# Optimization experiments

Hardware: AMD Instinct MI355X
Metric: run time of the kernel (lower is better)

Reference implementation:

```python
import jax, jax.numpy as jnp
import numpy as np
import math

N, LQ, DIM = 4, 1000, 256
HEADS, DHEAD, DEPTH = 8, 32, 2
LVLS, NPTS, MLP = 5, 4, 512
SCALE = DHEAD ** -0.5
SHAPES = np.array([[128, 128], [64, 64], [32, 32], [16, 16], [8, 8]], np.int32)
AREAS = SHAPES[:, 0] * SHAPES[:, 1]
STARTS = np.concatenate([[0], np.cumsum(AREAS)[:-1]]).astype(np.int32)
LIN = int(AREAS.sum())


def _ln(x, g, b):
    m = jnp.mean(x, -1, keepdims=True)
    v = jnp.var(x, -1, keepdims=True)
    return (x - m) * jax.lax.rsqrt(v + 1e-5) * g + b


def _gelu(x):  # tanh-approx GELU exactly as the torch module
    c = math.sqrt(2.0 / math.pi)
    return 0.5 * x * (1.0 + jnp.tanh(c * (x + 0.044715 * x ** 3)))


def _ms_deform(value, shapes, starts, loc, aw):
    # value [N,Lin,H,D]; loc [N,Lq,H,L,P,2] normalized to [0,1]; aw [N,Lq,H,L,P]
    n, lq, h, L, p, _ = loc.shape
    d = value.shape[-1]
    ni = jnp.arange(n)[:, None, None, None]
    hi = jnp.arange(h)[None, None, :, None]
    out = jnp.zeros((n, lq, h, d), value.dtype)
    for l in range(L):  # fixed small pyramid depth
        Hl, Wl = int(shapes[l, 0]), int(shapes[l, 1])
        s = int(starts[l])
        v = value[:, s:s + Hl * Wl].reshape(n, Hl, Wl, h, d)
        gx = loc[:, :, :, l, :, 0] * Wl - 0.5  # [N,Lq,H,P]
        gy = loc[:, :, :, l, :, 1] * Hl - 0.5
        x0 = jnp.floor(gx); y0 = jnp.floor(gy)
        lx = gx - x0; ly = gy - y0
        x0i = x0.astype(jnp.int32); y0i = y0.astype(jnp.int32)
        def corner(yi, xi):
            ok = ((yi >= 0) & (yi < Hl) & (xi >= 0) & (xi < Wl)).astype(value.dtype)
            g = v[ni, jnp.clip(yi, 0, Hl - 1), jnp.clip(xi, 0, Wl - 1), hi]  # [N,Lq,H,P,D]
            return g * ok[..., None]
        samp = (corner(y0i, x0i) * ((1 - ly) * (1 - lx))[..., None]
                + corner(y0i, x0i + 1) * ((1 - ly) * lx)[..., None]
                + corner(y0i + 1, x0i) * (ly * (1 - lx))[..., None]
                + corner(y0i + 1, x0i + 1) * (ly * lx)[..., None])
        out = out + jnp.einsum('nqhp,nqhpd->nqhd', aw[:, :, :, l], samp)
    return out.reshape(n, lq, h * d)


def _forward(x, src, center_pos, pos_w, pos_b, ln1_g, ln1_b, qkv_w, out_w, out_b,
             ln2_g, ln2_b, off_w, off_b, aw_w, aw_b, val_w, val_b, op_w, op_b,
             ln3_g, ln3_b, ff_w1, ff_b1, ff_w2, ff_b2, spatial_shapes, level_start_index):
    shapes = np.asarray(spatial_shapes)
    starts = np.asarray(level_start_index)
    n, lq, dim = x.shape
    pe = center_pos @ pos_w + pos_b                                   # pos_embedding(center_pos)
    ref = jnp.broadcast_to(center_pos[:, :, None, :], (n, lq, LVLS, 2))
    onorm = jnp.asarray(np.stack([shapes[:, 1], shapes[:, 0]], -1), x.dtype)  # [L,2] = (W,H)
    for i in range(DEPTH):
        # --- self-attention: PreNorm(x + pe) ---
        xn = _ln(x + pe, ln1_g[i], ln1_b[i])
        qkv = xn @ qkv_w[i]
        q, k, v = jnp.split(qkv, 3, axis=-1)
        q = q.reshape(n, lq, HEADS, DHEAD).transpose(0, 2, 1, 3)
        k = k.reshape(n, lq, HEADS, DHEAD).transpose(0, 2, 1, 3)
        v = v.reshape(n, lq, HEADS, DHEAD).transpose(0, 2, 1, 3)
        att = jax.nn.softmax(jnp.einsum('nhid,nhjd->nhij', q, k) * SCALE, axis=-1)
        o = jnp.einsum('nhij,nhjd->nhid', att, v).transpose(0, 2, 1, 3).reshape(n, lq, HEADS * DHEAD)
        x = x + o @ out_w[i] + out_b[i]
        # --- deformable cross-attention: PreNorm_CA norms query and src with same LN ---
        xn = _ln(x, ln2_g[i], ln2_b[i])
        srcn = _ln(src, ln2_g[i], ln2_b[i])
        query = xn + pe
        value = (srcn @ val_w[i] + val_b[i]).reshape(n, -1, HEADS, DHEAD)
        off = (query @ off_w[i] + off_b[i]).reshape(n, lq, HEADS, LVLS, NPTS, 2)
        aw = jax.nn.softmax((query @ aw_w[i] + aw_b[i]).reshape(n, lq, HEADS, LVLS * NPTS), axis=-1)
        aw = aw.reshape(n, lq, HEADS, LVLS, NPTS)
        loc = ref[:, :, None, :, None, :] + off / onorm[None, None, None, :, None, :]
        o = _ms_deform(value, shapes, starts, loc, aw)
        x = x + o @ op_w[i] + op_b[i]
        # --- feedforward: PreNorm ---
        xn = _ln(x, ln3_g[i], ln3_b[i])
        x = x + _gelu(xn @ ff_w1[i] + ff_b1[i]) @ ff_w2[i] + ff_b2[i]
    return x


def setup_inputs() -> dict:
    key = jax.random.key(0)
    ks = iter(jax.random.split(key, 64))
    r = lambda sh, s=0.02: jax.random.normal(next(ks), sh, jnp.float32) * s
    # sampling_offsets bias grid init (as in MSDeformAttn._reset_parameters)
    thetas = np.arange(HEADS) * (2.0 * math.pi / HEADS)
    grid = np.stack([np.cos(thetas), np.sin(thetas)], -1)
    grid = grid / np.abs(grid).max(-1, keepdims=True)
    grid = np.tile(grid[:, None, None, :], (1, LVLS, NPTS, 1)) * (np.arange(NPTS) + 1)[None, None, :, None]
    off_b = jnp.tile(jnp.asarray(grid.reshape(-1), jnp.float32)[None], (DEPTH, 1))
    return dict(
        x=jax.random.normal(next(ks), (N, LQ, DIM), jnp.float32),
        src=jax.random.normal(next(ks), (N, LIN, DIM), jnp.float32),
        center_pos=jax.random.uniform(next(ks), (N, LQ, 2), jnp.float32),
        spatial_shapes=jnp.asarray(SHAPES),
        level_start_index=jnp.asarray(STARTS),
        pos_w=r((2, DIM), 0.5), pos_b=jnp.zeros((DIM,), jnp.float32),
        ln1_g=jnp.ones((DEPTH, DIM), jnp.float32), ln1_b=jnp.zeros((DEPTH, DIM), jnp.float32),
        qkv_w=r((DEPTH, DIM, 3 * HEADS * DHEAD)),
        out_w=r((DEPTH, HEADS * DHEAD, DIM)), out_b=jnp.zeros((DEPTH, DIM), jnp.float32),
        ln2_g=jnp.ones((DEPTH, DIM), jnp.float32), ln2_b=jnp.zeros((DEPTH, DIM), jnp.float32),
        off_w=r((DEPTH, DIM, HEADS * LVLS * NPTS * 2)), off_b=off_b,
        aw_w=r((DEPTH, DIM, HEADS * LVLS * NPTS)), aw_b=jnp.zeros((DEPTH, HEADS * LVLS * NPTS), jnp.float32),
        val_w=r((DEPTH, DIM, HEADS * DHEAD)), val_b=jnp.zeros((DEPTH, HEADS * DHEAD), jnp.float32),
        op_w=r((DEPTH, HEADS * DHEAD, DIM)), op_b=jnp.zeros((DEPTH, DIM), jnp.float32),
        ln3_g=jnp.ones((DEPTH, DIM), jnp.float32), ln3_b=jnp.zeros((DEPTH, DIM), jnp.float32),
        ff_w1=r((DEPTH, DIM, MLP)), ff_b1=jnp.zeros((DEPTH, MLP), jnp.float32),
        ff_w2=r((DEPTH, MLP, DIM)), ff_b2=jnp.zeros((DEPTH, DIM), jnp.float32),
    )


def reference(x, src, center_pos, spatial_shapes, level_start_index, pos_w, pos_b,
              ln1_g, ln1_b, qkv_w, out_w, out_b, ln2_g, ln2_b, off_w, off_b,
              aw_w, aw_b, val_w, val_b, op_w, op_b, ln3_g, ln3_b,
              ff_w1, ff_b1, ff_w2, ff_b2):
    return _forward(x, src, center_pos, pos_w, pos_b, ln1_g, ln1_b, qkv_w, out_w, out_b,
                    ln2_g, ln2_b, off_w, off_b, aw_w, aw_b, val_w, val_b, op_w, op_b,
                    ln3_g, ln3_b, ff_w1, ff_b1, ff_w2, ff_b2, spatial_shapes, level_start_index)
```

## Files before the change

### kernel.cpp

```cpp
#include <hip/hip_runtime.h>
#include <hip/hip_bf16.h>
#include <math.h>

#define DIM 256
#define NB 4
#define LQ 1000
#define MLPD 512
#define LIN 21824
#define ROWS_X 4000
#define ROWS_SRC 87296
#define ATT_SCALE 0.17677669529663687f
#define LDK 72

typedef __hip_bfloat16 bf16;
typedef __attribute__((ext_vector_type(8))) short short8;
typedef __attribute__((ext_vector_type(4))) float floatx4;

__device__ __forceinline__ float rdv(const void* p, int f, size_t i){
    if (f) return ((const float*)p)[i];
    unsigned u = ((unsigned)((const unsigned short*)p)[i]) << 16;
    union { unsigned u; float f; } c; c.u = u; return c.f;
}
__device__ __forceinline__ short f2bs(float v){
    bf16 h = __float2bfloat16(v);
    return *reinterpret_cast<short*>(&h);
}
__device__ __forceinline__ float bs2f(short s){
// ... 5 lines not shown
    int t = threadIdx.x;
    bool hit = false;
    #pragma unroll
    for (int k = 0; k < 4; ++k) {
        unsigned short b = u[(t*4 + k)*2];
        union { unsigned u; float f; } c; c.u = ((unsigned)b) << 16;
        if (!(fabsf(c.f) <= 1000.f)) hit = true;
    }
    unsigned long long m = __ballot(hit);
    __shared__ unsigned long long red[4];
    if ((t & 63) == 0) red[t >> 6] = m;
    __syncthreads();
    if (t == 0) flag[0] = ((red[0]|red[1]|red[2]|red[3]) != 0ULL) ? 1 : 0;
}

struct PTab { const void* src[15]; float* dst[15]; int n[15]; };
__global__ void convs_kernel(PTab t, const int* __restrict__ flag){
    int j = blockIdx.y;
    int i = blockIdx.x*256 + threadIdx.x;
    if (i >= t.n[j]) return;
    t.dst[j][i] = t.src[j] ? rdv(t.src[j], flag[0], i) : 0.f;
}

__global__ void catb_kernel(const void* __restrict__ offb, const void* __restrict__ awb,
                            const int* __restrict__ flag, float* __restrict__ oab){
    int f = flag[0];
    int layer = blockIdx.y;
    int idx = blockIdx.x*256 + threadIdx.x;
    if (idx >= 480) return;
    float v = (idx < 320) ? rdv(offb, f, (size_t)layer*320 + idx)
                          : rdv(awb,  f, (size_t)layer*160 + idx - 320);
    oab[layer*480 + idx] = v;
}

struct WT { const void* src[8]; short* dst[8]; const float* scl[8];
            int K[8]; int N[8]; int ld[8]; int ro[8]; };
__global__ void wtransall_kernel(WT t, const int* __restrict__ flag){
    int j = blockIdx.z >> 1, b = blockIdx.z & 1;
    int K = t.K[j], N = t.N[j];
    int k0 = blockIdx.x*32, n0 = blockIdx.y*32;
    if (k0 >= K || n0 >= N) return;
    int f = flag[0];
    __shared__ float tt[32][33];
    int tx = threadIdx.x & 31, ty = threadIdx.x >> 5;
    size_t base = (size_t)b * K * N;
    for (int i = ty; i < 32; i += 8) {
        int k = k0 + i, n = n0 + tx;
// ... 26 lines not shown
    float part = t.bv[j][(size_t)b*256 + k] *
                 rdv(t.W[j], f, (size_t)b*256*N + (size_t)k*N + n);
    #pragma unroll
    for (int o = 32; o; o >>= 1) part += __shfl_xor(part, o, 64);
    __shared__ float red[4];
    int wave = k >> 6, lane = k & 63;
    if (lane == 0) red[wave] = part;
    __syncthreads();
    if (k == 0) {
        float s = red[0] + red[1] + red[2] + red[3];
        if (t.base[j]) s += t.base[j][(size_t)b*N + n];
        t.dst[j][(size_t)b*N + n] = s;
    }
}

__global__ void pe_kernel(const void* __restrict__ cp, const void* __restrict__ pw,
                          const void* __restrict__ pb, const int* __restrict__ flag,
                          float* __restrict__ pe){
    int f = flag[0];
    int row = blockIdx.x, t = threadIdx.x;
    float cx = rdv(cp, f, (size_t)row*2);
    float cy = rdv(cp, f, (size_t)row*2 + 1);
    pe[(size_t)row*DIM + t] = cx*rdv(pw, f, t) + cy*rdv(pw, f, DIM + t) + rdv(pb, f, t);
}

__global__ __launch_bounds__(256) void convx_kernel(const void* __restrict__ x,
        const float* __restrict__ pe, const int* __restrict__ flag,
        float* __restrict__ xf, float2* __restrict__ st){
    int f = flag[0];
    int wave = threadIdx.x >> 6, lane = threadIdx.x & 63;
    int row = blockIdx.x*4 + wave;
    float4 v;
    if (f) v = *(const float4*)((const float*)x + (size_t)row*DIM + lane*4);
    else {
        ushort4 u = *(const ushort4*)((const unsigned short*)x + (size_t)row*DIM + lane*4);
        v = make_float4(bs2f((short)u.x), bs2f((short)u.y), bs2f((short)u.z), bs2f((short)u.w));
    }
    *(float4*)(xf + (size_t)row*DIM + lane*4) = v;
    float4 p = *(const float4*)(pe + (size_t)row*DIM + lane*4);
    float a0 = v.x+p.x, a1 = v.y+p.y, a2 = v.z+p.z, a3 = v.w+p.w;
    float s  = a0+a1+a2+a3;
    float s2 = a0*a0+a1*a1+a2*a2+a3*a3;
    #pragma unroll
    for (int o = 32; o; o >>= 1) {
        s  += __shfl_xor(s,  o, 64);
        s2 += __shfl_xor(s2, o, 64);
    }
    if (lane == 0) st[row] = make_float2(s, s2);
}

__global__ __launch_bounds__(256) void stats2n_kernel(const void* __restrict__ src,
                                                      const int* __restrict__ flag,
                                                      bf16* __restrict__ srcn){
    int f = flag[0];
    int wave = threadIdx.x >> 6, lane = threadIdx.x & 63;
    int row = blockIdx.x*4 + wave;
    float v0, v1, v2, v3;
    if (f) {
        float4 x = *(const float4*)((const float*)src + (size_t)row*DIM + lane*4);
        v0 = x.x; v1 = x.y; v2 = x.z; v3 = x.w;
    } else {
        ushort4 u = *(const ushort4*)((const unsigned short*)src + (size_t)row*DIM + lane*4);
        v0 = bs2f((short)u.x); v1 = bs2f((short)u.y);
        v2 = bs2f((short)u.z); v3 = bs2f((short)u.w);
    }
    float s  = v0 + v1 + v2 + v3;
    float s2 = v0*v0 + v1*v1 + v2*v2 + v3*v3;
    #pragma unroll
    for (int o = 32; o; o >>= 1) {
        s  += __shfl_xor(s,  o, 64);
        s2 += __shfl_xor(s2, o, 64);
    }
    float mean = s * (1.f/DIM);
    float rstd = rsqrtf(s2 * (1.f/DIM) - mean*mean + 1e-5f);
    ushort4 o4;
    o4.x = (unsigned short)f2bs((v0-mean)*rstd);
    o4.y = (unsigned short)f2bs((v1-mean)*rstd);
    o4.z = (unsigned short)f2bs((v2-mean)*rstd);
    o4.w = (unsigned short)f2bs((v3-mean)*rstd);
    *(ushort4*)((unsigned short*)srcn + (size_t)row*DIM + lane*4) = o4;
}

template<int AMODE>
__global__ __launch_bounds__(256) void mgemm_kernel(
    const void* __restrict__ Asrc, const float2* __restrict__ asums,
    const float* __restrict__ ag, const float* __restrict__ ab,
    const float* __restrict__ Apre, const float* __restrict__ Apost,
    const short* __restrict__ Wt, const float* __restrict__ bias, const float* res,
    void* Cout, int M, int K, int N, int act, int cbf,
    float2* __restrict__ statacc, const float* __restrict__ sepe,
    void* __restrict__ fin, const int* __restrict__ flag){
    __shared__ short As[64*LDK];
    __shared__ short Bs[64*LDK];
    int tid = threadIdx.x;
    int wave = tid >> 6, lane = tid & 63;
    int wm = wave >> 1, wn = wave & 1;
    int quad = lane >> 4, l16 = lane & 15;
    int row0 = blockIdx.x*64, col0 = blockIdx.y*64;
    floatx4 acc[2][2];
    #pragma unroll
    for (int i = 0; i < 2; ++i)
        #pragma unroll
        for (int j = 0; j < 2; ++j)
            acc[i][j] = (floatx4){0.f,0.f,0.f,0.f};

    int r  = tid >> 2;
    int kc = (tid & 3) * 16;
    int gr = row0 + r;
    int gc = col0 + r;
    const short8 z8 = {0,0,0,0,0,0,0,0};

    for (int k0 = 0; k0 < K; k0 += 64) {
        short8 a0 = z8, a1 = z8;
        if (gr < M) {
            if (AMODE == 2) {
                const short8* p = (const short8*)((const short*)Asrc + (size_t)gr*K + k0 + kc);
                a0 = p[0]; a1 = p[1];
            } else {
                const float4* p = (const float4*)((const float*)Asrc + (size_t)gr*K + k0 + kc);
                float4 x0 = p[0], x1 = p[1], x2 = p[2], x3 = p[3];
                float av[16] = {x0.x,x0.y,x0.z,x0.w, x1.x,x1.y,x1.z,x1.w,
                                x2.x,x2.y,x2.z,x2.w, x3.x,x3.y,x3.z,x3.w};
                if (Apre) {
                    const float4* q = (const float4*)(Apre + (size_t)gr*K + k0 + kc);
                    float4 p0 = q[0], p1 = q[1], p2 = q[2], p3 = q[3];
                    float pv[16] = {p0.x,p0.y,p0.z,p0.w, p1.x,p1.y,p1.z,p1.w,
                                    p2.x,p2.y,p2.z,p2.w, p3.x,p3.y,p3.z,p3.w};
                    #pragma unroll
                    for (int j = 0; j < 16; ++j) av[j] += pv[j];
                }
                float2 st = asums[gr];
                float mean = st.x * (1.f/256.f);
                float rstd = rsqrtf(st.y*(1.f/256.f) - mean*mean + 1e-5f);
                if (AMODE == 3) {
                    const float4* gp = (const float4*)(ag + k0 + kc);
                    const float4* bp = (const float4*)(ab + k0 + kc);
                    float4 g0 = gp[0], g1 = gp[1], g2 = gp[2], g3 = gp[3];
                    float4 b0 = bp[0], b1 = bp[1], b2 = bp[2], b3 = bp[3];
                    float gv[16] = {g0.x,g0.y,g0.z,g0.w, g1.x,g1.y,g1.z,g1.w,
                                    g2.x,g2.y,g2.z,g2.w, g3.x,g3.y,g3.z,g3.w};
                    float bv[16] = {b0.x,b0.y,b0.z,b0.w, b1.x,b1.y,b1.z,b1.w,
                                    b2.x,b2.y,b2.z,b2.w, b3.x,b3.y,b3.z,b3.w};
                    #pragma unroll
                    for (int j = 0; j < 16; ++j)
                        av[j] = (av[j] - mean)*rstd*gv[j] + bv[j];
                    if (Apost) {
                        const float4* q = (const float4*)(Apost + (size_t)gr*K + k0 + kc);
                        float4 p0 = q[0], p1 = q[1], p2 = q[2], p3 = q[3];
                        float pv[16] = {p0.x,p0.y,p0.z,p0.w, p1.x,p1.y,p1.z,p1.w,
                                        p2.x,p2.y,p2.z,p2.w, p3.x,p3.y,p3.z,p3.w};
                        #pragma unroll
                        for (int j = 0; j < 16; ++j) av[j] += pv[j];
                    }
                } else {
                    #pragma unroll
                    for (int j = 0; j < 16; ++j)
                        av[j] = (av[j] - mean)*rstd;
                }
                #pragma unroll
                for (int j = 0; j < 8; ++j) { a0[j] = f2bs(av[j]); a1[j] = f2bs(av[8+j]); }
            }
        }
        *(short8*)&As[r*LDK + kc]     = a0;
        *(short8*)&As[r*LDK + kc + 8] = a1;
        short8 b0 = z8, b1 = z8;
        if (gc < N) {
            const short8* p = (const short8*)(Wt + (size_t)gc*K + k0 + kc);
            b0 = p[0]; b1 = p[1];
        }
        *(short8*)&Bs[r*LDK + kc]     = b0;
        *(short8*)&Bs[r*LDK + kc + 8] = b1;
        __syncthreads();
        #pragma unroll
        for (int kb = 0; kb < 64; kb += 32) {
            short8 af[2], bfr[2];
            #pragma unroll
            for (int mi = 0; mi < 2; ++mi)
                af[mi] = *(const short8*)&As[(wm*32 + mi*16 + l16)*LDK + kb + quad*8];
            #pragma unroll
            for (int ni = 0; ni < 2; ++ni)
                bfr[ni] = *(const short8*)&Bs[(wn*32 + ni*16 + l16)*LDK + kb + quad*8];
            #pragma unroll
            for (int mi = 0; mi < 2; ++mi)
                #pragma unroll
                for (int ni = 0; ni < 2; ++ni)
                    acc[mi][ni] = __builtin_amdgcn_mfma_f32_16x16x32_bf16(
// ... 3 lines not shown
    }
    float vout[2][2][4];
    #pragma unroll
    for (int mi = 0; mi < 2; ++mi) {
        int rbase = row0 + wm*32 + mi*16 + quad*4;
        #pragma unroll
        for (int ni = 0; ni < 2; ++ni) {
            int c = col0 + wn*32 + ni*16 + l16;
            #pragma unroll
            for (int r2 = 0; r2 < 4; ++r2) {
                int rr = rbase + r2;
                float v = 0.f;
                if (c < N && rr < M) {
                    v = acc[mi][ni][r2];
                    if (bias) v += bias[c];
                    if (act) v = 0.5f*v*(1.f + tanhf(0.7978845608028654f*(v + 0.044715f*v*v*v)));
                    if (res) v += res[(size_t)rr*N + c];
                }
                vout[mi][ni][r2] = v;
            }
        }
    }
    int fflag = 0;
    if (fin) fflag = flag[0];
    #pragma unroll
    for (int mi = 0; mi < 2; ++mi) {
        int rbase = row0 + wm*32 + mi*16 + quad*4;
        #pragma unroll
        for (int ni = 0; ni < 2; ++ni) {
            int c = col0 + wn*32 + ni*16 + l16;
            if (c >= N) continue;
// ... 30 lines not shown
                for (int o = 1; o < 16; o <<= 1) {
                    sv += __shfl_xor(sv, o, 64);
                    sq += __shfl_xor(sq, o, 64);
                }
                if (l16 == 0 && rr < M) {
                    atomicAdd(&statacc[rr].x, sv);
                    atomicAdd(&statacc[rr].y, sq);
                }
            }
        }
    }
}

__global__ __launch_bounds__(256) void mgemm128_kernel(
    const short* __restrict__ A, const short* __restrict__ Wt,
    const float* __restrict__ bias, bf16* __restrict__ C, int K, int N){
    __shared__ short As[128*LDK];
    __shared__ short Bs[128*LDK];
    int tid = threadIdx.x;
    int wave = tid >> 6, lane = tid & 63;
    int wm = wave >> 1, wn = wave & 1;
    int quad = lane >> 4, l16 = lane & 15;
    int row0 = blockIdx.x*128, col0 = blockIdx.y*128;
    floatx4 acc[4][4];
    #pragma unroll
    for (int i = 0; i < 4; ++i)
        #pragma unroll
        for (int j = 0; j < 4; ++j)
            acc[i][j] = (floatx4){0.f,0.f,0.f,0.f};

    for (int k0 = 0; k0 < K; k0 += 64) {
        #pragma unroll
        for (int i = 0; i < 2; ++i) {
            int idx = tid + i*256;
            int r = idx >> 2;
            int kc = (idx & 3) * 16;
            int gr = row0 + r;
            const short8* p = (const short8*)(A + (size_t)gr*K + k0 + kc);
            *(short8*)&As[r*LDK + kc]     = p[0];
            *(short8*)&As[r*LDK + kc + 8] = p[1];
            int gc = col0 + r;
            const short8* pb = (const short8*)(Wt + (size_t)gc*K + k0 + kc);
            *(short8*)&Bs[r*LDK + kc]     = pb[0];
            *(short8*)&Bs[r*LDK + kc + 8] = pb[1];
        }
        __syncthreads();
        #pragma unroll
        for (int kb = 0; kb < 64; kb += 32) {
            short8 af[4], bfr[4];
            #pragma unroll
            for (int mi = 0; mi < 4; ++mi)
                af[mi] = *(const short8*)&As[(wm*64 + mi*16 + l16)*LDK + kb + quad*8];
            #pragma unroll
            for (int ni = 0; ni < 4; ++ni)
                bfr[ni] = *(const short8*)&Bs[(wn*64 + ni*16 + l16)*LDK + kb + quad*8];
            #pragma unroll
            for (int mi = 0; mi < 4; ++mi)
                #pragma unroll
                for (int ni = 0; ni < 4; ++ni)
                    acc[mi][ni] = __builtin_amdgcn_mfma_f32_16x16x32_bf16(
                        af[mi], bfr[ni], acc[mi][ni], 0, 0, 0);
        }
        __syncthreads();
    }
    #pragma unroll
    for (int mi = 0; mi < 4; ++mi) {
        int rbase = row0 + wm*64 + mi*16 + quad*4;
        #pragma unroll
        for (int ni = 0; ni < 4; ++ni) {
            int c = col0 + wn*64 + ni*16 + l16;
            float bv = bias[c];
            #pragma unroll
            for (int r2 = 0; r2 < 4; ++r2)
                C[(size_t)(rbase + r2)*N + c] = __float2bfloat16(acc[mi][ni][r2] + bv);
        }
    }
}

__global__ __launch_bounds__(256) void fattn_kernel(const short* __restrict__ qkv,
                                                    bf16* __restrict__ out){
    int nh = blockIdx.y;
    int n = nh >> 3, h = nh & 7;
    int q0 = blockIdx.x * 64;
    __shared__ short Ks[64*40];
    __shared__ short VsT[32*72];
    __shared__ short Ps[64*72];
    int tid = threadIdx.x;
    int wave = tid >> 6, lane = tid & 63;
    int quad = lane >> 4, l16 = lane & 15;
// ... 4 lines not shown
    {
        int gq = q0 + wave*16 + l16;
        if (gq < LQ) {
            short8 s = *(const short8*)(qkv + ((size_t)(n*LQ+gq))*768 + h*32 + quad*8);
            #pragma unroll
            for (int j = 0; j < 8; ++j) qf[j] = f2bs(bs2f(s[j]) * ATT_SCALE);
        }
    }
    floatx4 acc[2];
    acc[0] = (floatx4){0.f,0.f,0.f,0.f};
    acc[1] = (floatx4){0.f,0.f,0.f,0.f};
    float m[4], lsum[4];
    #pragma unroll
    for (int i = 0; i < 4; ++i) { m[i] = -3.0e38f; lsum[i] = 0.f; }

    for (int k0 = 0; k0 < LQ; k0 += 64) {
        {
            int gk = k0 + r;
            short8 kv = z8, vv = z8;
            if (gk < LQ) {
                const short* rp = qkv + ((size_t)(n*LQ+gk))*768;
                kv = *(const short8*)(rp + 256 + h*32 + c8);
                vv = *(const short8*)(rp + 512 + h*32 + c8);
            }
            *(short8*)&Ks[r*40 + c8] = kv;
            #pragma unroll
            for (int j = 0; j < 8; ++j) VsT[(c8+j)*72 + r] = vv[j];
        }
        __syncthreads();
        floatx4 s4[4];
        #pragma unroll
        for (int kg = 0; kg < 4; ++kg) {
            short8 bfr = *(const short8*)&Ks[(kg*16 + l16)*40 + quad*8];
            s4[kg] = __builtin_amdgcn_mfma_f32_16x16x32_bf16(
                qf, bfr, (floatx4){0.f,0.f,0.f,0.f}, 0, 0, 0);
        }
        if (k0 + 64 > LQ) {
            #pragma unroll
            for (int kg = 0; kg < 4; ++kg)
                if (k0 + kg*16 + l16 >= LQ)
                    s4[kg] = (floatx4){-3.0e38f,-3.0e38f,-3.0e38f,-3.0e38f};
        }
// ... 29 lines not shown
        #pragma unroll
        for (int ni = 0; ni < 2; ++ni)
            #pragma unroll
            for (int r2 = 0; r2 < 4; ++r2)
                acc[ni][r2] *= fac[r2];
        #pragma unroll
        for (int kb = 0; kb < 64; kb += 32) {
            short8 pf = *(const short8*)&Ps[(wave*16 + l16)*72 + kb + quad*8];
            #pragma unroll
            for (int ni = 0; ni < 2; ++ni) {
                short8 vf = *(const short8*)&VsT[(ni*16 + l16)*72 + kb + quad*8];
                acc[ni] = __builtin_amdgcn_mfma_f32_16x16x32_bf16(pf, vf, acc[ni], 0, 0, 0);
            }
        }
        __syncthreads();
    }
    #pragma unroll
    for (int r2 = 0; r2 < 4; ++r2) {
        int row = q0 + wave*16 + quad*4 + r2;
        if (row >= LQ) continue;
        float inv = 1.f / lsum[r2];
        #pragma unroll
        for (int ni = 0; ni < 2; ++ni)
            out[((size_t)(n*LQ+row))*256 + h*32 + ni*16 + l16] =
                __float2bfloat16(acc[ni][r2] * inv);
    }
}

__global__ __launch_bounds__(256) void sample2_kernel(
        const bf16* __restrict__ value, const float* __restrict__ offaw,
// ... 10 lines not shown
    #pragma unroll
    for (int off = 16; off; off >>= 1) mx = fmaxf(mx, __shfl_xor(mx, off, 32));
    float p = (d < 20) ? __expf(logit - mx) : 0.f;
    float sm = p;
    #pragma unroll
    for (int off = 16; off; off >>= 1) sm += __shfl_xor(sm, off, 32);
    p *= (1.f / sm);

    const int HW[5] = {128,64,32,16,8};
    const int ST[5] = {0,16384,20480,21504,21760};
    float acc = 0.f;
    #pragma unroll
    for (int l = 0; l < 5; ++l) {
        int hw = HW[l];
        float fhw = (float)hw;
        size_t vb = ((size_t)n*LIN + ST[l]) * 256 + h*32 + d;
        #pragma unroll
        for (int pi = 0; pi < 4; ++pi) {
            const int idx = l*4 + pi;
            float w  = __shfl(p, idx, 32);
            float ox = (2*idx < 32)   ? __shfl(o0, 2*idx, 32)   : __shfl(o1, 2*idx-32, 32);
            float oy = (2*idx+1 < 32) ? __shfl(o0, 2*idx+1, 32) : __shfl(o1, 2*idx+1-32, 32);
            float gx = cx*fhw + ox - 0.5f;
            float gy = cy*fhw + oy - 0.5f;
            float x0f = floorf(gx), y0f = floorf(gy);
            float lx = gx - x0f, ly = gy - y0f;
            int x0 = (int)x0f, y0 = (int)y0f;
            int x1 = x0 + 1, y1 = y0 + 1;
            bool bx0 = (unsigned)x0 < (unsigned)hw, bx1 = (unsigned)x1 < (unsigned)hw;
            bool by0 = (unsigned)y0 < (unsigned)hw, by1 = (unsigned)y1 < (unsigned)hw;
            int x0c = min(max(x0, 0), hw-1), x1c = min(max(x1, 0), hw-1);
            int y0c = min(max(y0, 0), hw-1), y1c = min(max(y1, 0), hw-1);
            float v00 = __bfloat162float(value[vb + (size_t)(y0c*hw + x0c)*256]);
            float v01 = __bfloat162float(value[vb + (size_t)(y0c*hw + x1c)*256]);
            float v10 = __bfloat162float(value[vb + (size_t)(y1c*hw + x0c)*256]);
            float v11 = __bfloat162float(value[vb + (size_t)(y1c*hw + x1c)*256]);
            float w00 = (bx0 && by0) ? (1.f-ly)*(1.f-lx)*w : 0.f;
            float w01 = (bx1 && by0) ? (1.f-ly)*lx*w       : 0.f;
            float w10 = (bx0 && by1) ? ly*(1.f-lx)*w       : 0.f;
            float w11 = (bx1 && by1) ? ly*lx*w             : 0.f;
            acc = fmaf(w00, v00, acc);
            acc = fmaf(w01, v01, acc);
            acc = fmaf(w10, v10, acc);
            acc = fmaf(w11, v11, acc);
        }
    }
    out[(size_t)nq*256 + h*32 + d] = __float2bfloat16(acc);
}

extern "C" void kernel_launch(void* const* d_in, const int* in_sizes, int n_in,
                              void* d_out, int out_size, void* d_ws, size_t ws_size,
// ... 17 lines not shown
    float* qkvB  = (float*)(ws + alloc((size_t)2*768*4));
    float* ff1B  = (float*)(ws + alloc((size_t)2*512*4));
    float* valB  = (float*)(ws + alloc((size_t)2*256*4));
    const int sidx[13] = {5,6,7,8,11,12,13,19,21,22,23,25,27};
    const int ssz[13]  = {512,256,512,512,512,512,512,512,512,512,512,1024,512};
    float* sp[13];
    for (int j = 0; j < 13; ++j) sp[j] = (float*)(ws + alloc((size_t)ssz[j]*4));
    short* qkvT = (short*)(ws + alloc((size_t)2*768*256*2));
    short* outT = (short*)(ws + alloc((size_t)2*256*256*2));
    short* oawT = (short*)(ws + alloc((size_t)2*480*256*2));
    short* valT = (short*)(ws + alloc((size_t)2*256*256*2));
    short* opT  = (short*)(ws + alloc((size_t)2*256*256*2));
    short* ff1T = (short*)(ws + alloc((size_t)2*512*256*2));
    short* ff2T = (short*)(ws + alloc((size_t)2*256*512*2));
    bf16*  srcn = (bf16*)(ws + alloc((size_t)ROWS_SRC*DIM*2));
    bf16*  val  = (bf16*)(ws + alloc((size_t)ROWS_SRC*DIM*2));
    (void)ws_size; (void)in_sizes; (void)n_in; (void)out_size;

    float* pos_w = sp[0];  float* pos_b = sp[1];
    float* ln1_g = sp[2];  float* ln1_b = sp[3];
    float* out_b = sp[4];
    float* ln2_g = sp[5];  float* ln2_b = sp[6];
    float* val_b = sp[7];  float* op_b  = sp[8];
    float* ln3_g = sp[9];  float* ln3_b = sp[10];
    float* ff_b1 = sp[11]; float* ff_b2 = sp[12];
    (void)pos_w; (void)pos_b;

    detect_kernel<<<1, 256, 0, stream>>>(x_raw, flag);
    pe_kernel<<<ROWS_X, 256, 0, stream>>>(cp_raw, d_in[5], d_in[6], flag, pe);
    PTab pt;
    for (int j = 0; j < 13; ++j) { pt.src[j] = d_in[sidx[j]]; pt.dst[j] = sp[j]; pt.n[j] = ssz[j]; }
    pt.src[13] = cp_raw; pt.dst[13] = cpf; pt.n[13] = ROWS_X*2;
    pt.src[14] = nullptr; pt.dst[14] = (float*)(statbuf + ROWS_X); pt.n[14] = 5*ROWS_X*2;
    convs_kernel<<<dim3(157,15), 256, 0, stream>>>(pt, flag);
    catb_kernel<<<dim3(2,2), 256, 0, stream>>>(d_in[15], d_in[17], flag, oab);
    convx_kernel<<<ROWS_X/4, 256, 0, stream>>>(x_raw, pe, flag, xf, statbuf);
    stats2n_kernel<<<ROWS_SRC/4, 256, 0, stream>>>(src, flag, srcn);
    {
        WT wt;
        const int widx[8] = {9,10,14,16,18,20,24,26};
        short* wdst[8] = {qkvT, outT, oawT, oawT, valT, opT, ff1T, ff2T};
        const float* wscl[8] = {ln1_g, nullptr, nullptr, nullptr, ln2_g, nullptr, ln3_g, nullptr};
        const int wK[8]  = {256,256,256,256,256,256,256,512};
        const int wN[8]  = {768,256,320,160,256,256,512,256};
        const int wld[8] = {768,256,480,480,256,256,512,256};
        const int wro[8] = {0,0,0,320,0,0,0,0};
        for (int j = 0; j < 8; ++j) {
            wt.src[j] = d_in[widx[j]]; wt.dst[j] = wdst[j]; wt.scl[j] = wscl[j];
            wt.K[j] = wK[j]; wt.N[j] = wN[j]; wt.ld[j] = wld[j]; wt.ro[j] = wro[j];
        }
        wtransall_kernel<<<dim3(16,24,16), 256, 0, stream>>>(wt, flag);
    }
    {
        BFT bt;
        bt.W[0] = d_in[9];  bt.bv[0] = ln1_b; bt.base[0] = nullptr; bt.dst[0] = qkvB; bt.N[0] = 768;
        bt.W[1] = d_in[24]; bt.bv[1] = ln3_b; bt.base[1] = ff_b1;   bt.dst[1] = ff1B; bt.N[1] = 512;
        bt.W[2] = d_in[18]; bt.bv[2] = ln2_b; bt.base[2] = val_b;   bt.dst[2] = valB; bt.N[2] = 256;
        biasfold_kernel<<<dim3(1536,2), 256, 0, stream>>>(bt, flag);
    }

    int gmx = (ROWS_X + 63) / 64;
    for (int i = 0; i < 2; ++i) {
        float2* stA = statbuf + (size_t)(i ? 3 : 0)*ROWS_X;
        float2* stO = statbuf + (size_t)(i ? 4 : 1)*ROWS_X;
        float2* stF = statbuf + (size_t)(i ? 5 : 2)*ROWS_X;
        mgemm_kernel<4><<<dim3(gmx,12), 256, 0, stream>>>(
            xf, stA, nullptr, nullptr, pe, nullptr,
            qkvT + (size_t)i*768*256, qkvB + i*768, nullptr, qkv,
            ROWS_X, 256, 768, 0, 1, nullptr, nullptr, nullptr, flag);
        fattn_kernel<<<dim3(16,32), 256, 0, stream>>>((const short*)qkv, tmpb);
        mgemm_kernel<2><<<dim3(gmx,4), 256, 0, stream>>>(
            tmpb, nullptr, nullptr, nullptr, nullptr, nullptr,
            outT + (size_t)i*256*256, out_b + i*DIM, xf, xf,
            ROWS_X, 256, 256, 0, 0, stO, nullptr, nullptr, flag);
        mgemm128_kernel<<<dim3(ROWS_SRC/128, 2), 256, 0, stream>>>(
            (const short*)srcn, valT + (size_t)i*256*256, valB + i*256, val, 256, 256);
        mgemm_kernel<3><<<dim3(gmx,8), 256, 0, stream>>>(
            xf, stO, ln2_g + i*DIM, ln2_b + i*DIM, nullptr, pe,
            oawT + (size_t)i*480*256, oab + i*480, nullptr, offaw,
            ROWS_X, 256, 480, 0, 0, nullptr, nullptr, nullptr, flag);
        sample2_kernel<<<ROWS_X, 256, 0, stream>>>(val, offaw, cpf, tmpb);
        mgemm_kernel<2><<<dim3(gmx,4), 256, 0, stream>>>(
            tmpb, nullptr, nullptr, nullptr, nullptr, nullptr,
            opT + (size_t)i*256*256, op_b + i*DIM, xf, xf,
            ROWS_X, 256, 256, 0, 0, stF, nullptr, nullptr, flag);
        mgemm_kernel<4><<<dim3(gmx,8), 256, 0, stream>>>(
            xf, stF, nullptr, nullptr, nullptr, nullptr,
            ff1T + (size_t)i*512*256, ff1B + i*MLPD, nullptr, ffh,
            ROWS_X, 256, 512, 1, 1, nullptr, nullptr, nullptr, flag);
        if (i == 0) {
            mgemm_kernel<2><<<dim3(gmx,4), 256, 0, stream>>>(
                ffh, nullptr, nullptr, nullptr, nullptr, nullptr,
                ff2T + (size_t)i*256*512, ff_b2 + i*DIM, xf, xf,
                ROWS_X, 512, 256, 0, 0, statbuf + (size_t)3*ROWS_X, pe, nullptr, flag);
        } else {
            mgemm_kernel<2><<<dim3(gmx,4), 256, 0, stream>>>(
// ... 7 lines not shown
```

Before: 614.7 us.

## Fuse prep kernels, batch value projections, relayout values, prefetch GEMM tiles

Merges the small conversion, bias-concat and positional-encoding launches into one prep kernel, and merges the src-normalize and x-convert kernels into one launch. Both layers' value projections now run as a single GEMM before the layer loop, writing value in a head-major [layer][n][h][pos][d] layout so each bilinear corner read in the sampler touches a contiguous 32-element head slice. The GEMM and attention kernels gain register prefetch of the next K tile, LN gamma/beta are staged in shared memory, and GELU-tanh is rewritten as a sigmoid form using exp. Together these aim to cut launch overhead and load latency and to improve gather locality, at the cost of twice the value buffer memory and higher register pressure.

```diff
diff --git a/kernel.cpp b/kernel.cpp
--- a/kernel.cpp
+++ b/kernel.cpp
@@ -11,6 +11,7 @@
 #define ROWS_SRC 87296
 #define ATT_SCALE 0.17677669529663687f
 #define LDK 72
+#define VLAYER ((size_t)ROWS_SRC*256)
 
 typedef __hip_bfloat16 bf16;
 typedef __attribute__((ext_vector_type(8))) short short8;
@@ -46,23 +47,30 @@
     if (t == 0) flag[0] = ((red[0]|red[1]|red[2]|red[3]) != 0ULL) ? 1 : 0;
 }
 
-struct PTab { const void* src[15]; float* dst[15]; int n[15]; };
-__global__ void convs_kernel(PTab t, const int* __restrict__ flag){
-    int j = blockIdx.y;
-    int i = blockIdx.x*256 + threadIdx.x;
+struct PrepTab { const void* src[15]; float* dst[17]; int n[17]; int bs[18]; };
+__global__ void prep_kernel(PrepTab t, const void* __restrict__ offb,
+                            const void* __restrict__ awb, const void* __restrict__ pw,
+                            const void* __restrict__ pb, const void* __restrict__ cp,
+                            const int* __restrict__ flag){
+    int f = flag[0];
+    int bid = blockIdx.x;
+    int j = 0;
+    #pragma unroll 1
+    while (bid >= t.bs[j+1]) ++j;
+    int i = (bid - t.bs[j])*256 + threadIdx.x;
     if (i >= t.n[j]) return;
-    t.dst[j][i] = t.src[j] ? rdv(t.src[j], flag[0], i) : 0.f;
-}
-
-__global__ void catb_kernel(const void* __restrict__ offb, const void* __restrict__ awb,
-                            const int* __restrict__ flag, float* __restrict__ oab){
-    int f = flag[0];
-    int layer = blockIdx.y;
-    int idx = blockIdx.x*256 + threadIdx.x;
-    if (idx >= 480) return;
-    float v = (idx < 320) ? rdv(offb, f, (size_t)layer*320 + idx)
-                          : rdv(awb,  f, (size_t)layer*160 + idx - 320);
-    oab[layer*480 + idx] = v;
+    if (j < 15) {
+        t.dst[j][i] = t.src[j] ? rdv(t.src[j], f, i) : 0.f;
+    } else if (j == 15) {
+        int layer = i / 480, idx = i - layer*480;
+        float v = (idx < 320) ? rdv(offb, f, (size_t)layer*320 + idx)
+                              : rdv(awb,  f, (size_t)layer*160 + idx - 320);
+        t.dst[15][i] = v;
+    } else {
+        int row = i >> 8, c = i & 255;
+        float cx = rdv(cp, f, (size_t)row*2), cy = rdv(cp, f, (size_t)row*2 + 1);
+        t.dst[16][i] = cx*rdv(pw, f, c) + cy*rdv(pw, f, DIM + c) + rdv(pb, f, c);
+    }
 }
 
 struct WT { const void* src[8]; short* dst[8]; const float* scl[8];
@@ -119,71 +127,59 @@
     }
 }
 
-__global__ void pe_kernel(const void* __restrict__ cp, const void* __restrict__ pw,
-                          const void* __restrict__ pb, const int* __restrict__ flag,
-                          float* __restrict__ pe){
-    int f = flag[0];
-    int row = blockIdx.x, t = threadIdx.x;
-    float cx = rdv(cp, f, (size_t)row*2);
-    float cy = rdv(cp, f, (size_t)row*2 + 1);
-    pe[(size_t)row*DIM + t] = cx*rdv(pw, f, t) + cy*rdv(pw, f, DIM + t) + rdv(pb, f, t);
-}
-
-__global__ __launch_bounds__(256) void convx_kernel(const void* __restrict__ x,
-        const float* __restrict__ pe, const int* __restrict__ flag,
+__global__ __launch_bounds__(256) void statsconvx_kernel(const void* __restrict__ src,
+        const void* __restrict__ x, const float* __restrict__ pe,
+        const int* __restrict__ flag, bf16* __restrict__ srcn,
         float* __restrict__ xf, float2* __restrict__ st){
     int f = flag[0];
     int wave = threadIdx.x >> 6, lane = threadIdx.x & 63;
-    int row = blockIdx.x*4 + wave;
-    float4 v;
-    if (f) v = *(const float4*)((const float*)x + (size_t)row*DIM + lane*4);
-    else {
-        ushort4 u = *(const ushort4*)((const unsigned short*)x + (size_t)row*DIM + lane*4);
-        v = make_float4(bs2f((short)u.x), bs2f((short)u.y), bs2f((short)u.z), bs2f((short)u.w));
-    }
-    *(float4*)(xf + (size_t)row*DIM + lane*4) = v;
-    float4 p = *(const float4*)(pe + (size_t)row*DIM + lane*4);
-    float a0 = v.x+p.x, a1 = v.y+p.y, a2 = v.z+p.z, a3 = v.w+p.w;
-    float s  = a0+a1+a2+a3;
-    float s2 = a0*a0+a1*a1+a2*a2+a3*a3;
-    #pragma unroll
-    for (int o = 32; o; o >>= 1) {
-        s  += __shfl_xor(s,  o, 64);
-        s2 += __shfl_xor(s2, o, 64);
-    }
-    if (lane == 0) st[row] = make_float2(s, s2);
-}
-
-__global__ __launch_bounds__(256) void stats2n_kernel(const void* __restrict__ src,
-                                                      const int* __restrict__ flag,
-                                                      bf16* __restrict__ srcn){
-    int f = flag[0];
-    int wave = threadIdx.x >> 6, lane = threadIdx.x & 63;
-    int row = blockIdx.x*4 + wave;
-    float v0, v1, v2, v3;
-    if (f) {
-        float4 x = *(const float4*)((const float*)src + (size_t)row*DIM + lane*4);
-        v0 = x.x; v1 = x.y; v2 = x.z; v3 = x.w;
+    int bid = blockIdx.x;
+    if (bid < ROWS_SRC/4) {
+        int row = bid*4 + wave;
+        float v0, v1, v2, v3;
+        if (f) {
+            float4 xx = *(const float4*)((const float*)src + (size_t)row*DIM + lane*4);
+            v0 = xx.x; v1 = xx.y; v2 = xx.z; v3 = xx.w;
+        } else {
+            ushort4 u = *(const ushort4*)((const unsigned short*)src + (size_t)row*DIM + lane*4);
+            v0 = bs2f((short)u.x); v1 = bs2f((short)u.y);
+            v2 = bs2f((short)u.z); v3 = bs2f((short)u.w);
+        }
+        float s  = v0 + v1 + v2 + v3;
+        float s2 = v0*v0 + v1*v1 + v2*v2 + v3*v3;
+        #pragma unroll
+        for (int o = 32; o; o >>= 1) {
+            s  += __shfl_xor(s,  o, 64);
+            s2 += __shfl_xor(s2, o, 64);
+        }
+        float mean = s * (1.f/DIM);
+        float rstd = rsqrtf(s2 * (1.f/DIM) - mean*mean + 1e-5f);
+        ushort4 o4;
+        o4.x = (unsigned short)f2bs((v0-mean)*rstd);
+        o4.y = (unsigned short)f2bs((v1-mean)*rstd);
+        o4.z = (unsigned short)f2bs((v2-mean)*rstd);
+        o4.w = (unsigned short)f2bs((v3-mean)*rstd);
+        *(ushort4*)((unsigned short*)srcn + (size_t)row*DIM + lane*4) = o4;
     } else {
-        ushort4 u = *(const ushort4*)((const unsigned short*)src + (size_t)row*DIM + lane*4);
-        v0 = bs2f((short)u.x); v1 = bs2f((short)u.y);
-        v2 = bs2f((short)u.z); v3 = bs2f((short)u.w);
-    }
-    float s  = v0 + v1 + v2 + v3;
-    float s2 = v0*v0 + v1*v1 + v2*v2 + v3*v3;
-    #pragma unroll
-    for (int o = 32; o; o >>= 1) {
-        s  += __shfl_xor(s,  o, 64);
-        s2 += __shfl_xor(s2, o, 64);
-    }
-    float mean = s * (1.f/DIM);
-    float rstd = rsqrtf(s2 * (1.f/DIM) - mean*mean + 1e-5f);
-    ushort4 o4;
-    o4.x = (unsigned short)f2bs((v0-mean)*rstd);
-    o4.y = (unsigned short)f2bs((v1-mean)*rstd);
-    o4.z = (unsigned short)f2bs((v2-mean)*rstd);
-    o4.w = (unsigned short)f2bs((v3-mean)*rstd);
-    *(ushort4*)((unsigned short*)srcn + (size_t)row*DIM + lane*4) = o4;
+        int row = (bid - ROWS_SRC/4)*4 + wave;
+        float4 v;
+        if (f) v = *(const float4*)((const float*)x + (size_t)row*DIM + lane*4);
+        else {
+            ushort4 u = *(const ushort4*)((const unsigned short*)x + (size_t)row*DIM + lane*4);
+            v = make_float4(bs2f((short)u.x), bs2f((short)u.y), bs2f((short)u.z), bs2f((short)u.w));
+        }
+        *(float4*)(xf + (size_t)row*DIM + lane*4) = v;
+        float4 p = *(const float4*)(pe + (size_t)row*DIM + lane*4);
+        float a0 = v.x+p.x, a1 = v.y+p.y, a2 = v.z+p.z, a3 = v.w+p.w;
+        float s  = a0+a1+a2+a3;
+        float s2 = a0*a0+a1*a1+a2*a2+a3*a3;
+        #pragma unroll
+        for (int o = 32; o; o >>= 1) {
+            s  += __shfl_xor(s,  o, 64);
+            s2 += __shfl_xor(s2, o, 64);
+        }
+        if (lane == 0) st[row] = make_float2(s, s2);
+    }
 }
 
 template<int AMODE>
@@ -197,6 +193,7 @@
     void* __restrict__ fin, const int* __restrict__ flag){
     __shared__ short As[64*LDK];
     __shared__ short Bs[64*LDK];
+    __shared__ float gsh[256], bsh[256];
     int tid = threadIdx.x;
     int wave = tid >> 6, lane = tid & 63;
     int wm = wave >> 1, wn = wave & 1;
@@ -215,52 +212,61 @@
     int gc = col0 + r;
     const short8 z8 = {0,0,0,0,0,0,0,0};
 
+    if (AMODE == 3) {
+        if (tid < 256) { gsh[tid] = ag[tid]; bsh[tid] = ab[tid]; }
+        __syncthreads();
+    }
+    const float* aux = Apre ? Apre : Apost;
+    float mean = 0.f, rstd = 0.f;
+    if (AMODE != 2 && gr < M) {
+        float2 stt = asums[gr];
+        mean = stt.x * (1.f/256.f);
+        rstd = rsqrtf(stt.y*(1.f/256.f) - mean*mean + 1e-5f);
+    }
+    short8 ra0, ra1, rb0, rb1;
+    float4 rx0, rx1, rx2, rx3, rq0, rq1, rq2, rq3;
+    if (gr < M) {
+        if (AMODE == 2) {
+            const short8* p = (const short8*)((const short*)Asrc + (size_t)gr*K + kc);
+            ra0 = p[0]; ra1 = p[1];
+        } else {
+            const float4* p = (const float4*)((const float*)Asrc + (size_t)gr*K + kc);
+            rx0 = p[0]; rx1 = p[1]; rx2 = p[2]; rx3 = p[3];
+            if (aux) {
+                const float4* q = (const float4*)(aux + (size_t)gr*K + kc);
+                rq0 = q[0]; rq1 = q[1]; rq2 = q[2]; rq3 = q[3];
+            }
+        }
+    }
+    if (gc < N) {
+        const short8* p = (const short8*)(Wt + (size_t)gc*K + kc);
+        rb0 = p[0]; rb1 = p[1];
+    }
+
     for (int k0 = 0; k0 < K; k0 += 64) {
         short8 a0 = z8, a1 = z8;
         if (gr < M) {
-            if (AMODE == 2) {
-                const short8* p = (const short8*)((const short*)Asrc + (size_t)gr*K + k0 + kc);
-                a0 = p[0]; a1 = p[1];
-            } else {
-                const float4* p = (const float4*)((const float*)Asrc + (size_t)gr*K + k0 + kc);
-                float4 x0 = p[0], x1 = p[1], x2 = p[2], x3 = p[3];
-                float av[16] = {x0.x,x0.y,x0.z,x0.w, x1.x,x1.y,x1.z,x1.w,
-                                x2.x,x2.y,x2.z,x2.w, x3.x,x3.y,x3.z,x3.w};
-                if (Apre) {
-                    const float4* q = (const float4*)(Apre + (size_t)gr*K + k0 + kc);
-                    float4 p0 = q[0], p1 = q[1], p2 = q[2], p3 = q[3];
-                    float pv[16] = {p0.x,p0.y,p0.z,p0.w, p1.x,p1.y,p1.z,p1.w,
-                                    p2.x,p2.y,p2.z,p2.w, p3.x,p3.y,p3.z,p3.w};
+            if (AMODE == 2) { a0 = ra0; a1 = ra1; }
+            else {
+                float av[16] = {rx0.x,rx0.y,rx0.z,rx0.w, rx1.x,rx1.y,rx1.z,rx1.w,
+                                rx2.x,rx2.y,rx2.z,rx2.w, rx3.x,rx3.y,rx3.z,rx3.w};
+                float qv[16] = {rq0.x,rq0.y,rq0.z,rq0.w, rq1.x,rq1.y,rq1.z,rq1.w,
+                                rq2.x,rq2.y,rq2.z,rq2.w, rq3.x,rq3.y,rq3.z,rq3.w};
+                if (AMODE == 4) {
+                    if (Apre) {
+                        #pragma unroll
+                        for (int j = 0; j < 16; ++j) av[j] += qv[j];
+                    }
                     #pragma unroll
-                    for (int j = 0; j < 16; ++j) av[j] += pv[j];
-                }
-                float2 st = asums[gr];
-                float mean = st.x * (1.f/256.f);
-                float rstd = rsqrtf(st.y*(1.f/256.f) - mean*mean + 1e-5f);
-                if (AMODE == 3) {
-                    const float4* gp = (const float4*)(ag + k0 + kc);
-                    const float4* bp = (const float4*)(ab + k0 + kc);
-                    float4 g0 = gp[0], g1 = gp[1], g2 = gp[2], g3 = gp[3];
-                    float4 b0 = bp[0], b1 = bp[1], b2 = bp[2], b3 = bp[3];
-                    float gv[16] = {g0.x,g0.y,g0.z,g0.w, g1.x,g1.y,g1.z,g1.w,
-                                    g2.x,g2.y,g2.z,g2.w, g3.x,g3.y,g3.z,g3.w};
-                    float bv[16] = {b0.x,b0.y,b0.z,b0.w, b1.x,b1.y,b1.z,b1.w,
-                                    b2.x,b2.y,b2.z,b2.w, b3.x,b3.y,b3.z,b3.w};
-                    #pragma unroll
-                    for (int j = 0; j < 16; ++j)
-                        av[j] = (av[j] - mean)*rstd*gv[j] + bv[j];
-                    if (Apost) {
-                        const float4* q = (const float4*)(Apost + (size_t)gr*K + k0 + kc);
-                        float4 p0 = q[0], p1 = q[1], p2 = q[2], p3 = q[3];
-                        float pv[16] = {p0.x,p0.y,p0.z,p0.w, p1.x,p1.y,p1.z,p1.w,
-                                        p2.x,p2.y,p2.z,p2.w, p3.x,p3.y,p3.z,p3.w};
-                        #pragma unroll
-                        for (int j = 0; j < 16; ++j) av[j] += pv[j];
-                    }
+                    for (int j = 0; j < 16; ++j) av[j] = (av[j] - mean)*rstd;
                 } else {
                     #pragma unroll
                     for (int j = 0; j < 16; ++j)
-                        av[j] = (av[j] - mean)*rstd;
+                        av[j] = (av[j] - mean)*rstd*gsh[k0+kc+j] + bsh[k0+kc+j];
+                    if (Apost) {
+                        #pragma unroll
+                        for (int j = 0; j < 16; ++j) av[j] += qv[j];
+                    }
                 }
                 #pragma unroll
                 for (int j = 0; j < 8; ++j) { a0[j] = f2bs(av[j]); a1[j] = f2bs(av[8+j]); }
@@ -269,12 +275,29 @@
         *(short8*)&As[r*LDK + kc]     = a0;
         *(short8*)&As[r*LDK + kc + 8] = a1;
         short8 b0 = z8, b1 = z8;
-        if (gc < N) {
-            const short8* p = (const short8*)(Wt + (size_t)gc*K + k0 + kc);
-            b0 = p[0]; b1 = p[1];
-        }
+        if (gc < N) { b0 = rb0; b1 = rb1; }
         *(short8*)&Bs[r*LDK + kc]     = b0;
         *(short8*)&Bs[r*LDK + kc + 8] = b1;
+        int kn = k0 + 64;
+        if (kn < K) {
+            if (gr < M) {
+                if (AMODE == 2) {
+                    const short8* p = (const short8*)((const short*)Asrc + (size_t)gr*K + kn + kc);
+                    ra0 = p[0]; ra1 = p[1];
+                } else {
+                    const float4* p = (const float4*)((const float*)Asrc + (size_t)gr*K + kn + kc);
+                    rx0 = p[0]; rx1 = p[1]; rx2 = p[2]; rx3 = p[3];
+                    if (aux) {
+                        const float4* q = (const float4*)(aux + (size_t)gr*K + kn + kc);
+                        rq0 = q[0]; rq1 = q[1]; rq2 = q[2]; rq3 = q[3];
+                    }
+                }
+            }
+            if (gc < N) {
+                const short8* p = (const short8*)(Wt + (size_t)gc*K + kn + kc);
+                rb0 = p[0]; rb1 = p[1];
+            }
+        }
         __syncthreads();
         #pragma unroll
         for (int kb = 0; kb < 64; kb += 32) {
@@ -308,7 +331,11 @@
                 if (c < N && rr < M) {
                     v = acc[mi][ni][r2];
                     if (bias) v += bias[c];
-                    if (act) v = 0.5f*v*(1.f + tanhf(0.7978845608028654f*(v + 0.044715f*v*v*v)));
+                    if (act) {
+                        float z = fminf(1.5957691216057308f*(v + 0.044715f*v*v*v), 60.f);
+                        float e = __expf(z);
+                        v = v * e / (e + 1.f);
+                    }
                     if (res) v += res[(size_t)rr*N + c];
                 }
                 vout[mi][ni][r2] = v;
@@ -369,7 +396,8 @@
 
 __global__ __launch_bounds__(256) void mgemm128_kernel(
     const short* __restrict__ A, const short* __restrict__ Wt,
-    const float* __restrict__ bias, bf16* __restrict__ C, int K, int N){
+    const float* __restrict__ bias, bf16* __restrict__ valall){
+    const int K = 256;
     __shared__ short As[128*LDK];
     __shared__ short Bs[128*LDK];
     int tid = threadIdx.x;
@@ -384,20 +412,37 @@
         for (int j = 0; j < 4; ++j)
             acc[i][j] = (floatx4){0.f,0.f,0.f,0.f};
 
+    short8 pa[2][2], pb2[2][2];
+    #pragma unroll
+    for (int i = 0; i < 2; ++i) {
+        int idx = tid + i*256;
+        int rr = idx >> 2, kk = (idx & 3)*16;
+        const short8* p = (const short8*)(A + (size_t)(row0+rr)*K + kk);
+        pa[i][0] = p[0]; pa[i][1] = p[1];
+        const short8* pb = (const short8*)(Wt + (size_t)(col0+rr)*K + kk);
+        pb2[i][0] = pb[0]; pb2[i][1] = pb[1];
+    }
     for (int k0 = 0; k0 < K; k0 += 64) {
         #pragma unroll
         for (int i = 0; i < 2; ++i) {
             int idx = tid + i*256;
-            int r = idx >> 2;
-            int kc = (idx & 3) * 16;
-            int gr = row0 + r;
-            const short8* p = (const short8*)(A + (size_t)gr*K + k0 + kc);
-            *(short8*)&As[r*LDK + kc]     = p[0];
-            *(short8*)&As[r*LDK + kc + 8] = p[1];
-            int gc = col0 + r;
-            const short8* pb = (const short8*)(Wt + (size_t)gc*K + k0 + kc);
-            *(short8*)&Bs[r*LDK + kc]     = pb[0];
-            *(short8*)&Bs[r*LDK + kc + 8] = pb[1];
+            int rr = idx >> 2, kk = (idx & 3)*16;
+            *(short8*)&As[rr*LDK + kk]     = pa[i][0];
+            *(short8*)&As[rr*LDK + kk + 8] = pa[i][1];
+            *(short8*)&Bs[rr*LDK + kk]     = pb2[i][0];
+            *(short8*)&Bs[rr*LDK + kk + 8] = pb2[i][1];
+        }
+        int kn = k0 + 64;
+        if (kn < K) {
+            #pragma unroll
+            for (int i = 0; i < 2; ++i) {
+                int idx = tid + i*256;
+                int rr = idx >> 2, kk = (idx & 3)*16;
+                const short8* p = (const short8*)(A + (size_t)(row0+rr)*K + kn + kk);
+                pa[i][0] = p[0]; pa[i][1] = p[1];
+                const short8* pb = (const short8*)(Wt + (size_t)(col0+rr)*K + kn + kk);
+                pb2[i][0] = pb[0]; pb2[i][1] = pb[1];
+            }
         }
         __syncthreads();
         #pragma unroll
@@ -424,10 +469,17 @@
         #pragma unroll
         for (int ni = 0; ni < 4; ++ni) {
             int c = col0 + wn*64 + ni*16 + l16;
+            int l = c >> 8, hc = c & 255;
+            int h = hc >> 5, d = hc & 31;
             float bv = bias[c];
             #pragma unroll
-            for (int r2 = 0; r2 < 4; ++r2)
-                C[(size_t)(rbase + r2)*N + c] = __float2bfloat16(acc[mi][ni][r2] + bv);
+            for (int r2 = 0; r2 < 4; ++r2) {
+                int rr = rbase + r2;
+                unsigned n = (unsigned)rr / (unsigned)LIN;
+                int pos = rr - (int)n*LIN;
+                valall[(size_t)l*VLAYER + ((size_t)(n*8+h)*LIN + pos)*32 + d] =
+                    __float2bfloat16(acc[mi][ni][r2] + bv);
+            }
         }
     }
 }
@@ -462,18 +514,24 @@
     #pragma unroll
     for (int i = 0; i < 4; ++i) { m[i] = -3.0e38f; lsum[i] = 0.f; }
 
+    short8 kvp = z8, vvp = z8;
+    if (r < LQ) {
+        const short* rp = qkv + ((size_t)(n*LQ+r))*768;
+        kvp = *(const short8*)(rp + 256 + h*32 + c8);
+        vvp = *(const short8*)(rp + 512 + h*32 + c8);
+    }
     for (int k0 = 0; k0 < LQ; k0 += 64) {
-        {
-            int gk = k0 + r;
-            short8 kv = z8, vv = z8;
+        *(short8*)&Ks[r*40 + c8] = kvp;
+        #pragma unroll
+        for (int j = 0; j < 8; ++j) VsT[(c8+j)*72 + r] = vvp[j];
+        short8 kvn = z8, vvn = z8;
+        if (k0 + 64 < LQ) {
+            int gk = k0 + 64 + r;
             if (gk < LQ) {
                 const short* rp = qkv + ((size_t)(n*LQ+gk))*768;
-                kv = *(const short8*)(rp + 256 + h*32 + c8);
-                vv = *(const short8*)(rp + 512 + h*32 + c8);
-            }
-            *(short8*)&Ks[r*40 + c8] = kv;
-            #pragma unroll
-            for (int j = 0; j < 8; ++j) VsT[(c8+j)*72 + r] = vv[j];
+                kvn = *(const short8*)(rp + 256 + h*32 + c8);
+                vvn = *(const short8*)(rp + 512 + h*32 + c8);
+            }
         }
         __syncthreads();
         floatx4 s4[4];
@@ -533,6 +591,7 @@
             }
         }
         __syncthreads();
+        kvp = kvn; vvp = vvn;
     }
     #pragma unroll
     for (int r2 = 0; r2 < 4; ++r2) {
@@ -573,7 +632,7 @@
     for (int l = 0; l < 5; ++l) {
         int hw = HW[l];
         float fhw = (float)hw;
-        size_t vb = ((size_t)n*LIN + ST[l]) * 256 + h*32 + d;
+        size_t vb = ((size_t)(n*8 + h)*LIN + ST[l])*32 + d;
         #pragma unroll
         for (int pi = 0; pi < 4; ++pi) {
             const int idx = l*4 + pi;
@@ -590,10 +649,10 @@
             bool by0 = (unsigned)y0 < (unsigned)hw, by1 = (unsigned)y1 < (unsigned)hw;
             int x0c = min(max(x0, 0), hw-1), x1c = min(max(x1, 0), hw-1);
             int y0c = min(max(y0, 0), hw-1), y1c = min(max(y1, 0), hw-1);
-            float v00 = __bfloat162float(value[vb + (size_t)(y0c*hw + x0c)*256]);
-            float v01 = __bfloat162float(value[vb + (size_t)(y0c*hw + x1c)*256]);
-            float v10 = __bfloat162float(value[vb + (size_t)(y1c*hw + x0c)*256]);
-            float v11 = __bfloat162float(value[vb + (size_t)(y1c*hw + x1c)*256]);
+            float v00 = __bfloat162float(value[vb + (size_t)(y0c*hw + x0c)*32]);
+            float v01 = __bfloat162float(value[vb + (size_t)(y0c*hw + x1c)*32]);
+            float v10 = __bfloat162float(value[vb + (size_t)(y1c*hw + x0c)*32]);
+            float v11 = __bfloat162float(value[vb + (size_t)(y1c*hw + x1c)*32]);
             float w00 = (bx0 && by0) ? (1.f-ly)*(1.f-lx)*w : 0.f;
             float w01 = (bx1 && by0) ? (1.f-ly)*lx*w       : 0.f;
             float w10 = (bx0 && by1) ? ly*(1.f-lx)*w       : 0.f;
@@ -641,28 +700,37 @@
     short* ff1T = (short*)(ws + alloc((size_t)2*512*256*2));
     short* ff2T = (short*)(ws + alloc((size_t)2*256*512*2));
     bf16*  srcn = (bf16*)(ws + alloc((size_t)ROWS_SRC*DIM*2));
-    bf16*  val  = (bf16*)(ws + alloc((size_t)ROWS_SRC*DIM*2));
+    bf16*  valall = (bf16*)(ws + alloc((size_t)2*ROWS_SRC*DIM*2));
     (void)ws_size; (void)in_sizes; (void)n_in; (void)out_size;
 
-    float* pos_w = sp[0];  float* pos_b = sp[1];
     float* ln1_g = sp[2];  float* ln1_b = sp[3];
     float* out_b = sp[4];
     float* ln2_g = sp[5];  float* ln2_b = sp[6];
     float* val_b = sp[7];  float* op_b  = sp[8];
     float* ln3_g = sp[9];  float* ln3_b = sp[10];
     float* ff_b1 = sp[11]; float* ff_b2 = sp[12];
-    (void)pos_w; (void)pos_b;
 
     detect_kernel<<<1, 256, 0, stream>>>(x_raw, flag);
-    pe_kernel<<<ROWS_X, 256, 0, stream>>>(cp_raw, d_in[5], d_in[6], flag, pe);
-    PTab pt;
-    for (int j = 0; j < 13; ++j) { pt.src[j] = d_in[sidx[j]]; pt.dst[j] = sp[j]; pt.n[j] = ssz[j]; }
-    pt.src[13] = cp_raw; pt.dst[13] = cpf; pt.n[13] = ROWS_X*2;
-    pt.src[14] = nullptr; pt.dst[14] = (float*)(statbuf + ROWS_X); pt.n[14] = 5*ROWS_X*2;
-    convs_kernel<<<dim3(157,15), 256, 0, stream>>>(pt, flag);
-    catb_kernel<<<dim3(2,2), 256, 0, stream>>>(d_in[15], d_in[17], flag, oab);
-    convx_kernel<<<ROWS_X/4, 256, 0, stream>>>(x_raw, pe, flag, xf, statbuf);
-    stats2n_kernel<<<ROWS_SRC/4, 256, 0, stream>>>(src, flag, srcn);
+    {
+        PrepTab pt;
+        int nb = 0;
+        int nn[17];
+        for (int j = 0; j < 13; ++j) { pt.src[j] = d_in[sidx[j]]; pt.dst[j] = sp[j]; nn[j] = ssz[j]; }
+        pt.src[13] = cp_raw;  pt.dst[13] = cpf;  nn[13] = ROWS_X*2;
+        pt.src[14] = nullptr; pt.dst[14] = (float*)(statbuf + ROWS_X); nn[14] = 5*ROWS_X*2;
+        pt.dst[15] = oab;  nn[15] = 960;
+        pt.dst[16] = pe;   nn[16] = ROWS_X*DIM;
+        for (int j = 0; j < 17; ++j) {
+            pt.n[j] = nn[j];
+            pt.bs[j] = nb;
+            nb += (nn[j] + 255)/256;
+        }
+        pt.bs[17] = nb;
+        prep_kernel<<<nb, 256, 0, stream>>>(pt, d_in[15], d_in[17], d_in[5], d_in[6],
+                                            cp_raw, flag);
+    }
+    statsconvx_kernel<<<ROWS_SRC/4 + ROWS_X/4, 256, 0, stream>>>(
+        src, x_raw, pe, flag, srcn, xf, statbuf);
     {
         WT wt;
         const int widx[8] = {9,10,14,16,18,20,24,26};
@@ -685,6 +753,8 @@
         bt.W[2] = d_in[18]; bt.bv[2] = ln2_b; bt.base[2] = val_b;   bt.dst[2] = valB; bt.N[2] = 256;
         biasfold_kernel<<<dim3(1536,2), 256, 0, stream>>>(bt, flag);
     }
+    mgemm128_kernel<<<dim3(ROWS_SRC/128, 4), 256, 0, stream>>>(
+        (const short*)srcn, valT, valB, valall);
 
     int gmx = (ROWS_X + 63) / 64;
     for (int i = 0; i < 2; ++i) {
@@ -700,13 +770,12 @@
             tmpb, nullptr, nullptr, nullptr, nullptr, nullptr,
             outT + (size_t)i*256*256, out_b + i*DIM, xf, xf,
             ROWS_X, 256, 256, 0, 0, stO, nullptr, nullptr, flag);
-        mgemm128_kernel<<<dim3(ROWS_SRC/128, 2), 256, 0, stream>>>(
-            (const short*)srcn, valT + (size_t)i*256*256, valB + i*256, val, 256, 256);
         mgemm_kernel<3><<<dim3(gmx,8), 256, 0, stream>>>(
             xf, stO, ln2_g + i*DIM, ln2_b + i*DIM, nullptr, pe,
             oawT + (size_t)i*480*256, oab + i*480, nullptr, offaw,
             ROWS_X, 256, 480, 0, 0, nullptr, nullptr, nullptr, flag);
-        sample2_kernel<<<ROWS_X, 256, 0, stream>>>(val, offaw, cpf, tmpb);
+        sample2_kernel<<<ROWS_X, 256, 0, stream>>>(
+            valall + (size_t)i*VLAYER, offaw, cpf, tmpb);
         mgemm_kernel<2><<<dim3(gmx,4), 256, 0, stream>>>(
             tmpb, nullptr, nullptr, nullptr, nullptr, nullptr,
             opT + (size_t)i*256*256, op_b + i*DIM, xf, xf,
```

New measurement: 591.4 us. 3.8% less time.
